# Optimization experiments

Measured on AMD Instinct MI355X. Metric: run time of the kernel, lower is better.

Reference implementation:

```python
import jax, jax.numpy as jnp
import numpy as np

PATCH = 7
STRIDE = 1
ALPHA = 0.05


def extract_patches(im, p=PATCH, s=STRIDE):
    # im: (b, c, h, w) -> (b, n_patches, c*p*p)
    pat = jax.lax.conv_general_dilated_patches(im, (p, p), (s, s), 'VALID')  # (b, c*p*p, H', W')
    b, d = pat.shape[0], pat.shape[1]
    return pat.reshape(b, d, -1).transpose(0, 2, 1)


def _coherence_l2(xp, yp):
    # xp: (Ni, d) input patches, yp: (Nt, d) target patches, both fp16
    d = xp.shape[-1]
    x2 = jnp.sum(xp * xp, axis=-1)                     # (Ni,)
    y2 = jnp.sum(yp * yp, axis=-1)                     # (Nt,)
    cross = jnp.einsum('td,id->ti', yp, xp)            # (Nt, Ni)
    dist = (y2[:, None] + x2[None, :] - 2.0 * cross) / d
    # normalize each target row by its NN distance (+alpha), then min over targets
    dist = dist / (jnp.min(dist, axis=1, keepdims=True) + jnp.asarray(ALPHA, dist.dtype))
    return jnp.min(dist, axis=0).mean()


def setup_inputs() -> dict:
    key = jax.random.key(0)
    k1, k2 = jax.random.split(key)
    x = jax.random.normal(k1, (2, 3, 96, 96), dtype=jnp.float32)
    y = jax.random.normal(k2, (2, 3, 96, 96), dtype=jnp.float32)
    return {"x": x, "y": y}


def reference(x, y):
    x16 = x.astype(jnp.float16)
    y16 = y.astype(jnp.float16)
    xp = extract_patches(x16)   # (b, N, d)
    yp = extract_patches(y16)   # (b, N, d)
    per_image = jax.vmap(_coherence_l2)(xp, yp)  # (b,)
    return per_image.mean()
```

## Files before the change

### kernel.cpp

```cpp
#include <hip/hip_runtime.h>
#include <hip/hip_fp16.h>

#define IMGS 2
#define OW 90
#define NP 8100
#define HW 96
#define CH_STRIDE 9216
#define IMG_STRIDE 27648
#define KP 192
#define MP 8192
#define ALPHA 0.05f
#define INV_D (1.0f/147.0f)
#define PAD_SENTINEL 60000.0f

typedef _Float16 half8 __attribute__((ext_vector_type(8)));
typedef float floatx4 __attribute__((ext_vector_type(4)));

#define GLD_LDS16(gp, lp)                                                     \
    __builtin_amdgcn_global_load_lds(                                         \
        (const __attribute__((address_space(1))) void*)(gp),                  \
        (__attribute__((address_space(3))) void*)(lp), 16, 0, 0)

#define XP_OFF   0
#define YP_OFF   (XP_OFF + IMGS*MP*KP*2)
#define N2Y_OFF  (YP_OFF + IMGS*MP*KP*2)
#define RMIN_OFF (N2Y_OFF + IMGS*MP*4)
#define RINV_OFF (RMIN_OFF + IMGS*MP*4)
#define AY_OFF   (RINV_OFF + IMGS*MP*4)
#define CMIN_OFF (AY_OFF + IMGS*MP*4)

__global__ __launch_bounds__(256) void k_build(const float* __restrict__ x,
                                               const float* __restrict__ y,
                                               char* __restrict__ wsb) {
    int tid = threadIdx.x;
    int hwv = tid >> 5;
    int l = tid & 31;
    int grow = blockIdx.x * 8 + hwv;
    int tensor = grow >> 14;
    int img = (grow >> 13) & 1;
    int row = grow & (MP - 1);
    const float* src = (tensor ? y : x) + img * IMG_STRIDE;
    int py = row / OW, px = row - py * OW;
    bool rvalid = row < NP;

    float vals[8];
#pragma unroll
    for (int j = 0; j < 8; j++) {
        int k = l * 8 + j;
        float v = 0.0f;
        if (rvalid && k < 147) {
            int c = k / 49;
            int rm = k - c * 49;
            int dy = rm / 7, dx = rm - dy * 7;
            v = src[c * CH_STRIDE + (py + dy) * HW + px + dx];
        }
        vals[j] = (float)(_Float16)v;
    }
    float ss16 = 0.0f;
#pragma unroll
    for (int j = 0; j < 8; j++) ss16 = fmaf(vals[j], vals[j], ss16);
#pragma unroll
    for (int m = 1; m < 32; m <<= 1) ss16 += __shfl_xor(ss16, m, 32);

    if (tensor && l == 0)
        ((float*)(wsb + N2Y_OFF))[img * MP + row] = rvalid ? ss16 : 0.0f;

    half8 h;
#pragma unroll
    for (int j = 0; j < 8; j++) {
        float f = vals[j];
        if (tensor) f *= -2.0f;
        h[j] = (_Float16)f;
    }
    if (l == 18) {
        h[3] = tensor ? (_Float16)1.0f
                      : (rvalid ? (_Float16)ss16 : (_Float16)PAD_SENTINEL);
    }
    if (l < 24) {
        _Float16* dst = (_Float16*)(wsb + (tensor ? YP_OFF : XP_OFF)) +
                        ((size_t)img * MP + row) * KP + l * 8;
        *(half8*)dst = h;
    }
    if (tid < 8) {
        int gi = blockIdx.x * 8 + tid;
        if (gi < IMGS * MP)
            ((int*)(wsb + RMIN_OFF))[gi] = 0x7f800000;
        else
            ((int*)(wsb + CMIN_OFF))[gi - IMGS * MP] = 0x7f800000;
    }
}

template <int PASS>
__global__ __launch_bounds__(256, 2) void k_gemm(char* __restrict__ wsb) {
    __shared__ __align__(16) _Float16 B0r1[128 * 128];
    __shared__ __align__(16) _Float16 B0r2[128 * 32];
    __shared__ __align__(16) _Float16 B1r1[128 * 128];
    __shared__ __align__(16) _Float16 B1r2[128 * 32];
    int tid = threadIdx.x;
    int lane = tid & 63, w = tid >> 6;
    int wm = (w >> 1) * 64, wn = (w & 1) * 64;
    int quad = lane >> 4, col16 = lane & 15;
    int q = blockIdx.x;
    int rtile = blockIdx.y;
    int img = blockIdx.z;

    const _Float16* Res = (const _Float16*)(wsb + (PASS == 1 ? YP_OFF : XP_OFF)) +
                          ((size_t)img * MP + rtile * 128) * KP;
    const _Float16* Str = (const _Float16*)(wsb + (PASS == 1 ? XP_OFF : YP_OFF)) +
                          (size_t)img * MP * KP;

    int roff1 = lane >> 4, cc1 = lane & 15;
    int roff2 = lane >> 2, cc2 = lane & 3;
#define STAGE(Mat, R1, R2)                                                     \
    {                                                                          \
        int rbase = w * 32;                                                    \
        _Pragma("unroll") for (int g = 0; g < 8; g++) {                        \
            int r = rbase + g * 4 + roff1;                                     \
            int gc = cc1 ^ (r & 7);                                            \
            GLD_LDS16((Mat) + (size_t)r * KP + gc * 8, &(R1)[(rbase + g * 4) * 128]); \
        }                                                                      \
        _Pragma("unroll") for (int g = 0; g < 2; g++) {                        \
            int r = rbase + g * 16 + roff2;                                    \
            int gc = cc2 ^ ((r >> 1) & 3);                                     \
            GLD_LDS16((Mat) + (size_t)r * KP + 128 + gc * 8, &(R2)[(rbase + g * 16) * 32]); \
        }                                                                      \
    }

#define READFRAG(R1, R2, row, ks)                                              \
    ((ks) < 4 ? *(const half8*)(&(R1)[(row) * 128 + ((((ks) * 4 + quad) ^ ((row) & 7)) * 8)]) \
              : *(const half8*)(&(R2)[(row) * 32 + ((quad ^ (((row) >> 1) & 3)) * 8)]))

    STAGE(Res, B0r1, B0r2);
    __syncthreads();
    half8 rf[4][5];
    int rrow0 = (PASS == 1) ? wm : wn;
#pragma unroll
    for (int i = 0; i < 4; i++)
#pragma unroll
        for (int c = 0; c < 5; c++)
            rf[i][c] = READFRAG(B0r1, B0r2, rrow0 + i * 16 + col16, c);
    __syncthreads();
    STAGE(Str + (size_t)(q * 16) * 128 * KP, B0r1, B0r2);

    float rmin[4][4];
    float cmin[4];
#pragma unroll
    for (int i = 0; i < 4; i++) {
        cmin[i] = 1e30f;
#pragma unroll
        for (int j = 0; j < 4; j++) rmin[i][j] = 1e30f;
    }
    int srow0 = (PASS == 1) ? wn : wm;
    const float* RIp = (const float*)(wsb + RINV_OFF) + img * MP;
    const float* AYp = (const float*)(wsb + AY_OFF) + img * MP;

    for (int s = 0; s < 16; s++) {
        __syncthreads();
        const _Float16* R1 = (s & 1) ? B1r1 : B0r1;
        const _Float16* R2 = (s & 1) ? B1r2 : B0r2;
        if (s < 15) {
            _Float16* W1 = (s & 1) ? B0r1 : B1r1;
            _Float16* W2 = (s & 1) ? B0r2 : B1r2;
            const _Float16* M = Str + (size_t)(q * 16 + s + 1) * 128 * KP;
            STAGE(M, W1, W2);
        }
        float rr[4][4], aa[4][4];
        if (PASS == 2) {
            int rgb = (q * 16 + s) * 128 + wm + quad * 4;
#pragma unroll
            for (int mi = 0; mi < 4; mi++)
#pragma unroll
                for (int r = 0; r < 4; r++) {
                    rr[mi][r] = RIp[rgb + mi * 16 + r];
                    aa[mi][r] = AYp[rgb + mi * 16 + r];
                }
        }
        floatx4 acc[4][4];
#pragma unroll
        for (int i = 0; i < 4; i++)
#pragma unroll
            for (int j = 0; j < 4; j++) acc[i][j] = (floatx4){0.f, 0.f, 0.f, 0.f};
#pragma unroll
        for (int ks = 0; ks < 5; ks++) {
            half8 sf[4];
#pragma unroll
            for (int i = 0; i < 4; i++)
                sf[i] = READFRAG(R1, R2, srow0 + i * 16 + col16, ks);
#pragma unroll
            for (int mi = 0; mi < 4; mi++)
#pragma unroll
                for (int ni = 0; ni < 4; ni++)
                    acc[mi][ni] = __builtin_amdgcn_mfma_f32_16x16x32_f16(
                        (PASS == 1) ? rf[mi][ks] : sf[mi],
                        (PASS == 1) ? sf[ni] : rf[ni][ks],
                        acc[mi][ni], 0, 0, 0);
        }
        if (PASS == 1) {
#pragma unroll
            for (int mi = 0; mi < 4; mi++)
#pragma unroll
                for (int r = 0; r < 4; r++) {
                    float m4 = fminf(fminf(acc[mi][0][r], acc[mi][1][r]),
                                     fminf(acc[mi][2][r], acc[mi][3][r]));
                    rmin[mi][r] = fminf(rmin[mi][r], m4);
                }
        } else {
#pragma unroll
            for (int mi = 0; mi < 4; mi++)
#pragma unroll
                for (int r = 0; r < 4; r++) {
#pragma unroll
                    for (int ni = 0; ni < 4; ni++)
                        cmin[ni] = fminf(cmin[ni],
                                         fmaf(rr[mi][r], acc[mi][ni][r], aa[mi][r]));
                }
        }
    }

    if (PASS == 1) {
#pragma unroll
        for (int mi = 0; mi < 4; mi++)
#pragma unroll
            for (int r = 0; r < 4; r++) {
                float best = rmin[mi][r];
                best = fminf(best, __shfl_xor(best, 1, 16));
                best = fminf(best, __shfl_xor(best, 2, 16));
                best = fminf(best, __shfl_xor(best, 4, 16));
                best = fminf(best, __shfl_xor(best, 8, 16));
                int rg = rtile * 128 + wm + mi * 16 + quad * 4 + r;
                if (col16 == 0 && rg < NP)
                    atomicMin((int*)(wsb + RMIN_OFF) + img * MP + rg,
                              __float_as_int(best));
            }
    } else {
#pragma unroll
        for (int ni = 0; ni < 4; ni++) {
            float best = cmin[ni];
            best = fminf(best, __shfl_xor(best, 16, 64));
            best = fminf(best, __shfl_xor(best, 32, 64));
            if (quad == 0)
                atomicMin((int*)(wsb + CMIN_OFF) + img * MP +
                              rtile * 128 + wn + ni * 16 + col16,
                          __float_as_int(best));
        }
    }
}

__global__ __launch_bounds__(256) void k_rinv(char* __restrict__ wsb) {
    int gid = blockIdx.x * 256 + threadIdx.x;
    float rm = __int_as_float(((const int*)(wsb + RMIN_OFF))[gid]);
    float y2 = ((const float*)(wsb + N2Y_OFF))[gid];
    float d = (y2 + rm) * INV_D;
    float rp = INV_D / (d + ALPHA);
    bool valid = (gid & (MP - 1)) < NP;
    ((float*)(wsb + RINV_OFF))[gid] = valid ? rp : 0.0f;
    ((float*)(wsb + AY_OFF))[gid] = valid ? rp * y2 : __builtin_huge_valf();
}

__global__ __launch_bounds__(256) void k_final(const char* __restrict__ wsb,
                                               float* __restrict__ out) {
    __shared__ float red[256];
    int tid = threadIdx.x;
    const int* cm = (const int*)(wsb + CMIN_OFF);
    float s = 0.0f;
    for (int i = tid; i < NP; i += 256) {
        s += __int_as_float(cm[i]);
        s += __int_as_float(cm[MP + i]);
    }
    red[tid] = s;
    __syncthreads();
    for (int st = 128; st > 0; st >>= 1) {
        if (tid < st) red[tid] += red[tid + st];
        __syncthreads();
    }
    if (tid == 0) out[0] = red[0] * (0.5f / NP);
}

extern "C" void kernel_launch(void* const* d_in, const int* in_sizes, int n_in,
                              void* d_out, int out_size, void* d_ws, size_t ws_size,
                              hipStream_t stream) {
    const float* x = (const float*)d_in[0];
    const float* y = (const float*)d_in[1];
    char* wsb = (char*)d_ws;
    float* out = (float*)d_out;

    k_build<<<4096, 256, 0, stream>>>(x, y, wsb);
    k_gemm<1><<<dim3(4, 64, IMGS), 256, 0, stream>>>(wsb);
    k_rinv<<<(IMGS * MP) / 256, 256, 0, stream>>>(wsb);
    k_gemm<2><<<dim3(4, 64, IMGS), 256, 0, stream>>>(wsb);
    k_final<<<1, 256, 0, stream>>>(wsb, out);
}
```

Before: 170.6 us.

## Drop LDS double buffering, halve per-block stream tiles, stage row scales in LDS

Result: slower. 264.9 us (+55.3%).

```diff
diff --git a/kernel.cpp b/kernel.cpp
--- a/kernel.cpp
+++ b/kernel.cpp
@@ -91,11 +91,11 @@
 }
 
 template <int PASS>
-__global__ __launch_bounds__(256, 2) void k_gemm(char* __restrict__ wsb) {
-    __shared__ __align__(16) _Float16 B0r1[128 * 128];
-    __shared__ __align__(16) _Float16 B0r2[128 * 32];
-    __shared__ __align__(16) _Float16 B1r1[128 * 128];
-    __shared__ __align__(16) _Float16 B1r2[128 * 32];
+__global__ __launch_bounds__(256, 3) void k_gemm(char* __restrict__ wsb) {
+    __shared__ __align__(16) _Float16 R1[128 * 128];
+    __shared__ __align__(16) _Float16 R2[128 * 32];
+    __shared__ float rsld[128];
+    __shared__ float ayld[128];
     int tid = threadIdx.x;
     int lane = tid & 63, w = tid >> 6;
     int wm = (w >> 1) * 64, wn = (w & 1) * 64;
@@ -111,26 +111,26 @@
 
     int roff1 = lane >> 4, cc1 = lane & 15;
     int roff2 = lane >> 2, cc2 = lane & 3;
-#define STAGE(Mat, R1, R2)                                                     \
+#define STAGE(Mat)                                                             \
     {                                                                          \
         int rbase = w * 32;                                                    \
         _Pragma("unroll") for (int g = 0; g < 8; g++) {                        \
             int r = rbase + g * 4 + roff1;                                     \
             int gc = cc1 ^ (r & 7);                                            \
-            GLD_LDS16((Mat) + (size_t)r * KP + gc * 8, &(R1)[(rbase + g * 4) * 128]); \
+            GLD_LDS16((Mat) + (size_t)r * KP + gc * 8, &R1[(rbase + g * 4) * 128]); \
         }                                                                      \
         _Pragma("unroll") for (int g = 0; g < 2; g++) {                        \
             int r = rbase + g * 16 + roff2;                                    \
             int gc = cc2 ^ ((r >> 1) & 3);                                     \
-            GLD_LDS16((Mat) + (size_t)r * KP + 128 + gc * 8, &(R2)[(rbase + g * 16) * 32]); \
+            GLD_LDS16((Mat) + (size_t)r * KP + 128 + gc * 8, &R2[(rbase + g * 16) * 32]); \
         }                                                                      \
     }
 
-#define READFRAG(R1, R2, row, ks)                                              \
-    ((ks) < 4 ? *(const half8*)(&(R1)[(row) * 128 + ((((ks) * 4 + quad) ^ ((row) & 7)) * 8)]) \
-              : *(const half8*)(&(R2)[(row) * 32 + ((quad ^ (((row) >> 1) & 3)) * 8)]))
-
-    STAGE(Res, B0r1, B0r2);
+#define READFRAG(row, ks)                                                      \
+    ((ks) < 4 ? *(const half8*)(&R1[(row) * 128 + ((((ks) * 4 + quad) ^ ((row) & 7)) * 8)]) \
+              : *(const half8*)(&R2[(row) * 32 + ((quad ^ (((row) >> 1) & 3)) * 8)]))
+
+    STAGE(Res);
     __syncthreads();
     half8 rf[4][5];
     int rrow0 = (PASS == 1) ? wm : wn;
@@ -138,9 +138,7 @@
     for (int i = 0; i < 4; i++)
 #pragma unroll
         for (int c = 0; c < 5; c++)
-            rf[i][c] = READFRAG(B0r1, B0r2, rrow0 + i * 16 + col16, c);
-    __syncthreads();
-    STAGE(Str + (size_t)(q * 16) * 128 * KP, B0r1, B0r2);
+            rf[i][c] = READFRAG(rrow0 + i * 16 + col16, c);
 
     float rmin[4][4];
     float cmin[4];
@@ -154,27 +152,15 @@
     const float* RIp = (const float*)(wsb + RINV_OFF) + img * MP;
     const float* AYp = (const float*)(wsb + AY_OFF) + img * MP;
 
-    for (int s = 0; s < 16; s++) {
+    for (int s = 0; s < 8; s++) {
         __syncthreads();
-        const _Float16* R1 = (s & 1) ? B1r1 : B0r1;
-        const _Float16* R2 = (s & 1) ? B1r2 : B0r2;
-        if (s < 15) {
-            _Float16* W1 = (s & 1) ? B0r1 : B1r1;
-            _Float16* W2 = (s & 1) ? B0r2 : B1r2;
-            const _Float16* M = Str + (size_t)(q * 16 + s + 1) * 128 * KP;
-            STAGE(M, W1, W2);
-        }
-        float rr[4][4], aa[4][4];
-        if (PASS == 2) {
-            int rgb = (q * 16 + s) * 128 + wm + quad * 4;
-#pragma unroll
-            for (int mi = 0; mi < 4; mi++)
-#pragma unroll
-                for (int r = 0; r < 4; r++) {
-                    rr[mi][r] = RIp[rgb + mi * 16 + r];
-                    aa[mi][r] = AYp[rgb + mi * 16 + r];
-                }
-        }
+        STAGE(Str + (size_t)(q * 8 + s) * 128 * KP);
+        if (PASS == 2 && tid < 128) {
+            int gr = (q * 8 + s) * 128 + tid;
+            rsld[tid] = RIp[gr];
+            ayld[tid] = AYp[gr];
+        }
+        __syncthreads();
         floatx4 acc[4][4];
 #pragma unroll
         for (int i = 0; i < 4; i++)
@@ -185,7 +171,7 @@
             half8 sf[4];
 #pragma unroll
             for (int i = 0; i < 4; i++)
-                sf[i] = READFRAG(R1, R2, srow0 + i * 16 + col16, ks);
+                sf[i] = READFRAG(srow0 + i * 16 + col16, ks);
 #pragma unroll
             for (int mi = 0; mi < 4; mi++)
 #pragma unroll
@@ -209,10 +195,13 @@
             for (int mi = 0; mi < 4; mi++)
 #pragma unroll
                 for (int r = 0; r < 4; r++) {
+                    int row_l = wm + mi * 16 + quad * 4 + r;
+                    float rr = rsld[row_l];
+                    float aa = ayld[row_l];
 #pragma unroll
                     for (int ni = 0; ni < 4; ni++)
                         cmin[ni] = fminf(cmin[ni],
-                                         fmaf(rr[mi][r], acc[mi][ni][r], aa[mi][r]));
+                                         fmaf(rr, acc[mi][ni][r], aa));
                 }
         }
     }
@@ -285,8 +274,8 @@
     float* out = (float*)d_out;
 
     k_build<<<4096, 256, 0, stream>>>(x, y, wsb);
-    k_gemm<1><<<dim3(4, 64, IMGS), 256, 0, stream>>>(wsb);
+    k_gemm<1><<<dim3(8, 64, IMGS), 256, 0, stream>>>(wsb);
     k_rinv<<<(IMGS * MP) / 256, 256, 0, stream>>>(wsb);
-    k_gemm<2><<<dim3(4, 64, IMGS), 256, 0, stream>>>(wsb);
+    k_gemm<2><<<dim3(8, 64, IMGS), 256, 0, stream>>>(wsb);
     k_final<<<1, 256, 0, stream>>>(wsb, out);
 }
```
